# Kernel optimization log

Hardware: AMD Instinct MI355X
Metric: run time of the kernel (lower is better)

## Reference

```python
import jax, jax.numpy as jnp
import numpy as np

D_IN = 6      # raw node feature dim (self_attn_init first arg)
D_INIT = 16   # init encoding dim (self_attn_init second arg)
D_CAT = 22    # 6 + 16 (self_attn_enc first arg)
D_ENC = 64    # encoding dim (self_attn_enc second arg / gated_aggr_attn)
N = 1024      # number of nodes in node_cloud


def setup_inputs() -> dict:
    key = jax.random.key(0)
    ks = jax.random.split(key, 8)
    return {
        "node_cloud": jax.random.normal(ks[0], (N, D_IN), jnp.float32),
        "Wq_i": jax.random.normal(ks[1], (D_IN, D_INIT), jnp.float32) / np.sqrt(D_IN),
        "Wk_i": jax.random.normal(ks[2], (D_IN, D_INIT), jnp.float32) / np.sqrt(D_IN),
        "Wv_i": jax.random.normal(ks[3], (D_IN, D_INIT), jnp.float32) / np.sqrt(D_IN),
        "Wq_e": jax.random.normal(ks[4], (D_IN, D_ENC), jnp.float32) / np.sqrt(D_IN),
        "Wk_e": jax.random.normal(ks[5], (D_CAT, D_ENC), jnp.float32) / np.sqrt(D_CAT),
        "Wv_e": jax.random.normal(ks[6], (D_CAT, D_ENC), jnp.float32) / np.sqrt(D_CAT),
        "wg": jax.random.normal(ks[7], (D_ENC,), jnp.float32) / np.sqrt(D_ENC),
        "bg": jnp.zeros((), jnp.float32),
    }


def reference(node_cloud, Wq_i, Wk_i, Wv_i, Wq_e, Wk_e, Wv_e, wg, bg):
    # Stage 1: self_attn_init, batched over all C=N centres at once.
    # Per centre c: attend over every node, per-node 16-d encoding.
    Q_i = node_cloud @ Wq_i                     # [C, 16] (one query per centre)
    K_i = node_cloud @ Wk_i                     # [N, 16]
    V_i = node_cloud @ Wv_i                     # [N, 16]
    scores_i = (Q_i @ K_i.T) / np.sqrt(D_INIT)  # [C, N]
    a_i = jax.nn.softmax(scores_i, axis=-1)     # [C, N]
    nce_init = a_i[:, :, None] * V_i[None]      # [C, N, 16]

    # Stage 2: self_attn_enc on concat(raw node feats, init encodings).
    x = jnp.concatenate(
        [jnp.broadcast_to(node_cloud[None], (N, N, D_IN)), nce_init], axis=-1
    )                                            # [C, N, 22]
    Q_e = node_cloud @ Wq_e                      # [C, 64]
    K_e = jnp.einsum("cnf,fd->cnd", x, Wk_e)     # [C, N, 64]
    V_e = jnp.einsum("cnf,fd->cnd", x, Wv_e)     # [C, N, 64]
    scores_e = jnp.einsum("cnd,cd->cn", K_e, Q_e) / np.sqrt(D_ENC)  # [C, N]
    a_e = jax.nn.softmax(scores_e, axis=-1)      # [C, N]
    enc = a_e[:, :, None] * V_e                  # [C, N, 64]

    # Stage 3: gated_aggr_attn over the node axis -> one 64-vector per centre.
    g = jax.nn.sigmoid(enc @ wg + bg)            # [C, N]
    out = jnp.einsum("cn,cnd->cd", g, enc)       # [C, 64]
    return out
```

## Files before the change

kernel.cpp:

```cpp
#include <hip/hip_runtime.h>
#include <math.h>

#define NN 1024
#define DE 64
#define DCAT 22
#define GC 2
#define NTC 512
#define NWAVE (NTC/64)
#define NBLK (NN/GC)

__device__ __forceinline__ float wave_sum(float v) {
    int t;
    t = __builtin_amdgcn_update_dpp(0, __float_as_int(v), 0x111, 0xf, 0xf, true); v += __int_as_float(t);
    t = __builtin_amdgcn_update_dpp(0, __float_as_int(v), 0x112, 0xf, 0xf, true); v += __int_as_float(t);
    t = __builtin_amdgcn_update_dpp(0, __float_as_int(v), 0x114, 0xf, 0xf, true); v += __int_as_float(t);
    t = __builtin_amdgcn_update_dpp(0, __float_as_int(v), 0x118, 0xf, 0xf, true); v += __int_as_float(t);
    t = __builtin_amdgcn_update_dpp(0, __float_as_int(v), 0x142, 0xf, 0xf, true); v += __int_as_float(t);
    t = __builtin_amdgcn_update_dpp(0, __float_as_int(v), 0x143, 0xf, 0xf, true); v += __int_as_float(t);
    return v;
}

__global__ __launch_bounds__(NTC, 4) void nce_fused(
    const float* __restrict__ nc,
    const float* __restrict__ Wq_i, const float* __restrict__ Wk_i,
    const float* __restrict__ Wv_i, const float* __restrict__ Wq_e,
    const float* __restrict__ Wk_e, const float* __restrict__ Wv_e,
    const float* __restrict__ wg,  const float* __restrict__ bgp,
    float* __restrict__ out)
{
    __shared__ float  s_wqi[96], s_wki[96], s_wvi[96], s_wg[64];
    __shared__ float  s_wqe[384], s_wke[1408], s_wve[1408];
    __shared__ float  s_M[6*DCAT], s_Mi[36], s_u[DCAT];
    __shared__ float  s_q[GC][32];
    __shared__ float2 s_red1[NWAVE], s_red2[NWAVE];
    __shared__ float2 s_acc[NWAVE][DCAT];
    __shared__ float  s_fin[DCAT*GC];

    const int tid  = threadIdx.x, wave = tid >> 6, lane = tid & 63;
    const int c0   = blockIdx.x * GC;
    const int nA   = tid, nB = tid + NTC;

    float xA[6], xB[6];
    #pragma unroll
    for (int f = 0; f < 6; ++f) { xA[f] = nc[nA*6 + f]; xB[f] = nc[nB*6 + f]; }

    if (tid < 96) { s_wqi[tid] = Wq_i[tid]; s_wki[tid] = Wk_i[tid]; s_wvi[tid] = Wv_i[tid]; }
    else if (tid >= 128 && tid < 192) s_wg[tid-128] = wg[tid-128];
    if (tid < 384) s_wqe[tid] = Wq_e[tid];
    for (int i = tid; i < 1408; i += NTC) { s_wke[i] = Wk_e[i]; s_wve[i] = Wv_e[i]; }
    __syncthreads();

    if (tid < 132) {
        const int f = tid % 6, k = tid / 6;
        float a = 0.f;
        #pragma unroll
        for (int d = 0; d < 64; ++d) a += s_wqe[f*64+d]*s_wke[k*64+d];
        s_M[f*DCAT+k] = a * 0.125f;
    } else if (tid < 168) {
        const int t = tid - 132, g = t % 6, f = t / 6;
        float a = 0.f;
        #pragma unroll
        for (int j = 0; j < 16; ++j) a += s_wqi[g*16+j]*s_wki[f*16+j];
        s_Mi[g*6+f] = a * 0.25f;
    } else if (tid < 190) {
        const int k = tid - 168;
        float a = 0.f;
        #pragma unroll
        for (int d = 0; d < 64; ++d) a += s_wve[k*64+d]*s_wg[d];
        s_u[k] = a;
    }
    __syncthreads();

    float viA[16], viB[16];
    #pragma unroll
    for (int j = 0; j < 16; ++j) {
        float a = 0.f, b = 0.f;
        #pragma unroll
        for (int f = 0; f < 6; ++f) { a += xA[f]*s_wvi[f*16+j]; b += xB[f]*s_wvi[f*16+j]; }
        viA[j] = a; viB[j] = b;
    }
    float grA = 0.f, grB = 0.f, gvA = 0.f, gvB = 0.f;
    #pragma unroll
    for (int f = 0; f < 6; ++f)  { grA += xA[f]*s_u[f];    grB += xB[f]*s_u[f]; }
    #pragma unroll
    for (int j = 0; j < 16; ++j) { gvA += viA[j]*s_u[6+j]; gvB += viB[j]*s_u[6+j]; }

    if (tid < GC*32) {
        const int c = tid >> 5, k = tid & 31;
        float xc[6];
        #pragma unroll
        for (int f = 0; f < 6; ++f) xc[f] = nc[(c0+c)*6 + f];
        float a = 0.f;
        if (k < 6) {
            #pragma unroll
            for (int g = 0; g < 6; ++g) a += xc[g]*s_Mi[g*6+k];
        } else if (k >= 8 && k < 14) {
            #pragma unroll
            for (int f = 0; f < 6; ++f) a += xc[f]*s_M[f*DCAT + (k-8)];
        } else if (k >= 16) {
            #pragma unroll
            for (int f = 0; f < 6; ++f) a += xc[f]*s_M[f*DCAT + 6 + (k-16)];
        }
        s_q[c][k] = a;
    }
    const float bg = *bgp;
    __syncthreads();

    float aiA[GC], aiB[GC];
    #pragma unroll
    for (int c = 0; c < GC; ++c) {
        const float* q = s_q[c];
        float sA = 0.f, sB = 0.f;
        #pragma unroll
        for (int f = 0; f < 6; ++f) { sA += q[f]*xA[f]; sB += q[f]*xB[f]; }
        aiA[c] = __expf(sA); aiB[c] = __expf(sB);
    }
    {
        float r0 = wave_sum(aiA[0]+aiB[0]);
        float r1 = wave_sum(aiA[1]+aiB[1]);
        if (lane == 63) s_red1[wave] = make_float2(r0, r1);
    }
    __syncthreads();
    {
        float2 dd = s_red1[0];
        #pragma unroll
        for (int w2 = 1; w2 < NWAVE; ++w2) { float2 t = s_red1[w2]; dd.x += t.x; dd.y += t.y; }
        float inv0 = 1.f/dd.x, inv1 = 1.f/dd.y;
        aiA[0] *= inv0; aiB[0] *= inv0; aiA[1] *= inv1; aiB[1] *= inv1;
    }

    float w1A[GC], w2A[GC], w1B[GC], w2B[GC];
    {
        float eA[GC], eB[GC];
        #pragma unroll
        for (int c = 0; c < GC; ++c) {
            const float* q = s_q[c];
            float uA = 0.f, uB = 0.f, vA = 0.f, vB = 0.f;
            #pragma unroll
            for (int f = 0; f < 6; ++f) { uA += q[8+f]*xA[f]; uB += q[8+f]*xB[f]; }
            #pragma unroll
            for (int j = 0; j < 16; ++j) { vA += q[16+j]*viA[j]; vB += q[16+j]*viB[j]; }
            eA[c] = __expf(uA + aiA[c]*vA);
            eB[c] = __expf(uB + aiB[c]*vB);
        }
        float s0 = wave_sum(eA[0]+eB[0]);
        float s1 = wave_sum(eA[1]+eB[1]);
        if (lane == 63) s_red2[wave] = make_float2(s0, s1);
        __syncthreads();
        float2 dd = s_red2[0];
        #pragma unroll
        for (int w2 = 1; w2 < NWAVE; ++w2) { float2 t = s_red2[w2]; dd.x += t.x; dd.y += t.y; }
        float den[GC] = {dd.x, dd.y};
        #pragma unroll
        for (int c = 0; c < GC; ++c) {
            float inv = 1.f/den[c];
            float aeA = eA[c]*inv, aeB = eB[c]*inv;
            float preA = aeA*(grA + aiA[c]*gvA) + bg;
            float preB = aeB*(grB + aiB[c]*gvB) + bg;
            float gA = 1.f/(1.f + __expf(-preA));
            float gB = 1.f/(1.f + __expf(-preB));
            w1A[c] = gA*aeA; w2A[c] = w1A[c]*aiA[c];
            w1B[c] = gB*aeB; w2B[c] = w1B[c]*aiB[c];
        }
    }

    #pragma unroll
    for (int f = 0; f < 6; ++f) {
        float a0 = wave_sum(w1A[0]*xA[f] + w1B[0]*xB[f]);
        float a1 = wave_sum(w1A[1]*xA[f] + w1B[1]*xB[f]);
        if (lane == 63) s_acc[wave][f] = make_float2(a0, a1);
    }
    #pragma unroll
    for (int j = 0; j < 16; ++j) {
        float a0 = wave_sum(w2A[0]*viA[j] + w2B[0]*viB[j]);
        float a1 = wave_sum(w2A[1]*viA[j] + w2B[1]*viB[j]);
        if (lane == 63) s_acc[wave][6+j] = make_float2(a0, a1);
    }
    __syncthreads();
    if (tid < DCAT*GC) {
        const int k = tid >> 1, c = tid & 1;
        float a = 0.f;
        #pragma unroll
        for (int w2 = 0; w2 < NWAVE; ++w2)
            a += ((const float*)&s_acc[w2][k])[c];
        s_fin[k*GC + c] = a;
    }
    __syncthreads();

    if (tid < GC*DE) {
        const int c = tid >> 6, d = tid & 63;
        float o = 0.f;
        #pragma unroll
        for (int k = 0; k < DCAT; ++k) o += s_fin[k*GC + c]*s_wve[k*64 + d];
        out[(c0 + c)*DE + d] = o;
    }
}

extern "C" void kernel_launch(void* const* d_in, const int* in_sizes, int n_in,
                              void* d_out, int out_size, void* d_ws, size_t ws_size,
                              hipStream_t stream)
{
    const float* nc   = (const float*)d_in[0];
    const float* Wq_i = (const float*)d_in[1];
    const float* Wk_i = (const float*)d_in[2];
    const float* Wv_i = (const float*)d_in[3];
    const float* Wq_e = (const float*)d_in[4];
    const float* Wk_e = (const float*)d_in[5];
    const float* Wv_e = (const float*)d_in[6];
    const float* wg   = (const float*)d_in[7];
    const float* bg   = (const float*)d_in[8];
    float* out = (float*)d_out;

    nce_fused<<<NBLK, NTC, 0, stream>>>(nc, Wq_i, Wk_i, Wv_i, Wq_e, Wk_e, Wv_e,
                                        wg, bg, out);
}
```

Baseline: 21.63 us.

## Split weight-product and per-node precompute into a prologue kernel

Adds a small pre-kernel that computes the folded weight matrices (M, Mi, u), a transposed copy of the node features and the per-node V_i values, and stores them in workspace. The main per-centre kernel then loads these instead of having every one of 512 blocks redo the weight products and V_i projection. It also switches the final reductions to 16-lane DPP sums with a wider shared partial array, and uses float4 reads of the query vectors. The cost is a second kernel launch and a serial dependency between the two kernels.

```diff
diff --git a/kernel.cpp b/kernel.cpp
--- a/kernel.cpp
+++ b/kernel.cpp
@@ -8,6 +8,12 @@
 #define NTC 512
 #define NWAVE (NTC/64)
 #define NBLK (NN/GC)
+
+#define OFF_M   0
+#define OFF_MI  132
+#define OFF_U   168
+#define OFF_XT  192
+#define OFF_VIT (OFF_XT + 6*NN)
 
 __device__ __forceinline__ float wave_sum(float v) {
     int t;
@@ -19,100 +25,125 @@
     t = __builtin_amdgcn_update_dpp(0, __float_as_int(v), 0x143, 0xf, 0xf, true); v += __int_as_float(t);
     return v;
 }
-
-__global__ __launch_bounds__(NTC, 4) void nce_fused(
+__device__ __forceinline__ float wave_sum16(float v) {
+    int t;
+    t = __builtin_amdgcn_update_dpp(0, __float_as_int(v), 0x111, 0xf, 0xf, true); v += __int_as_float(t);
+    t = __builtin_amdgcn_update_dpp(0, __float_as_int(v), 0x112, 0xf, 0xf, true); v += __int_as_float(t);
+    t = __builtin_amdgcn_update_dpp(0, __float_as_int(v), 0x114, 0xf, 0xf, true); v += __int_as_float(t);
+    t = __builtin_amdgcn_update_dpp(0, __float_as_int(v), 0x118, 0xf, 0xf, true); v += __int_as_float(t);
+    return v;
+}
+
+__global__ __launch_bounds__(256) void nce_pre(
     const float* __restrict__ nc,
     const float* __restrict__ Wq_i, const float* __restrict__ Wk_i,
     const float* __restrict__ Wv_i, const float* __restrict__ Wq_e,
     const float* __restrict__ Wk_e, const float* __restrict__ Wv_e,
-    const float* __restrict__ wg,  const float* __restrict__ bgp,
+    const float* __restrict__ wg, float* __restrict__ ws)
+{
+    __shared__ float s_wqi[96], s_wki[96], s_wvi[96], s_wg[64];
+    __shared__ float s_wqe[384], s_wke[1408], s_wve[1408];
+    const int tid = threadIdx.x, bid = blockIdx.x;
+    const int wv = tid >> 6, lane = tid & 63;
+
+    if (tid < 96) { s_wqi[tid] = Wq_i[tid]; s_wki[tid] = Wk_i[tid]; s_wvi[tid] = Wv_i[tid]; }
+    if (tid >= 96 && tid < 160) s_wg[tid-96] = wg[tid-96];
+    for (int i = tid; i < 384; i += 256) s_wqe[i] = Wq_e[i];
+    for (int i = tid; i < 1408; i += 256) { s_wke[i] = Wk_e[i]; s_wve[i] = Wv_e[i]; }
+    __syncthreads();
+
+    for (int e = bid*4 + wv; e < 190; e += 16) {
+        float p; int dst; float scale;
+        if (e < 132) {
+            const int f = e % 6, k = e / 6;
+            p = s_wqe[f*64 + lane] * s_wke[k*64 + lane];
+            dst = OFF_M + f*22 + k; scale = 0.125f;
+        } else if (e < 168) {
+            const int t = e - 132, g = t % 6, f = t / 6;
+            p = (lane < 16) ? s_wqi[g*16 + lane] * s_wki[f*16 + lane] : 0.f;
+            dst = OFF_MI + g*6 + f; scale = 0.25f;
+        } else {
+            const int k = e - 168;
+            p = s_wve[k*64 + lane] * s_wg[lane];
+            dst = OFF_U + k; scale = 1.f;
+        }
+        float ssum = wave_sum(p);
+        if (lane == 63) ws[dst] = ssum * scale;
+    }
+
+    const int n = bid*256 + tid;
+    float x[6];
+    #pragma unroll
+    for (int f = 0; f < 6; ++f) { x[f] = nc[n*6 + f]; ws[OFF_XT + f*NN + n] = x[f]; }
+    #pragma unroll
+    for (int j = 0; j < 16; ++j) {
+        float a = 0.f;
+        #pragma unroll
+        for (int f = 0; f < 6; ++f) a += x[f]*s_wvi[f*16 + j];
+        ws[OFF_VIT + j*NN + n] = a;
+    }
+}
+
+__global__ __launch_bounds__(NTC, 4) void nce_centre(
+    const float* __restrict__ ws, const float* __restrict__ nc,
+    const float* __restrict__ Wv_e, const float* __restrict__ bgp,
     float* __restrict__ out)
 {
-    __shared__ float  s_wqi[96], s_wki[96], s_wvi[96], s_wg[64];
-    __shared__ float  s_wqe[384], s_wke[1408], s_wve[1408];
-    __shared__ float  s_M[6*DCAT], s_Mi[36], s_u[DCAT];
-    __shared__ float  s_q[GC][32];
+    __shared__ float  s_c[192];
+    __shared__ float  s_wve[DCAT*DE];
+    __shared__ __align__(16) float s_q[GC][32];
     __shared__ float2 s_red1[NWAVE], s_red2[NWAVE];
-    __shared__ float2 s_acc[NWAVE][DCAT];
+    __shared__ float2 s_acc[32][DCAT];
     __shared__ float  s_fin[DCAT*GC];
 
-    const int tid  = threadIdx.x, wave = tid >> 6, lane = tid & 63;
-    const int c0   = blockIdx.x * GC;
-    const int nA   = tid, nB = tid + NTC;
-
-    float xA[6], xB[6];
-    #pragma unroll
-    for (int f = 0; f < 6; ++f) { xA[f] = nc[nA*6 + f]; xB[f] = nc[nB*6 + f]; }
-
-    if (tid < 96) { s_wqi[tid] = Wq_i[tid]; s_wki[tid] = Wk_i[tid]; s_wvi[tid] = Wv_i[tid]; }
-    else if (tid >= 128 && tid < 192) s_wg[tid-128] = wg[tid-128];
-    if (tid < 384) s_wqe[tid] = Wq_e[tid];
-    for (int i = tid; i < 1408; i += NTC) { s_wke[i] = Wk_e[i]; s_wve[i] = Wv_e[i]; }
-    __syncthreads();
-
-    if (tid < 132) {
-        const int f = tid % 6, k = tid / 6;
-        float a = 0.f;
-        #pragma unroll
-        for (int d = 0; d < 64; ++d) a += s_wqe[f*64+d]*s_wke[k*64+d];
-        s_M[f*DCAT+k] = a * 0.125f;
-    } else if (tid < 168) {
-        const int t = tid - 132, g = t % 6, f = t / 6;
-        float a = 0.f;
-        #pragma unroll
-        for (int j = 0; j < 16; ++j) a += s_wqi[g*16+j]*s_wki[f*16+j];
-        s_Mi[g*6+f] = a * 0.25f;
-    } else if (tid < 190) {
-        const int k = tid - 168;
-        float a = 0.f;
-        #pragma unroll
-        for (int d = 0; d < 64; ++d) a += s_wve[k*64+d]*s_wg[d];
-        s_u[k] = a;
-    }
-    __syncthreads();
-
-    float viA[16], viB[16];
-    #pragma unroll
-    for (int j = 0; j < 16; ++j) {
-        float a = 0.f, b = 0.f;
-        #pragma unroll
-        for (int f = 0; f < 6; ++f) { a += xA[f]*s_wvi[f*16+j]; b += xB[f]*s_wvi[f*16+j]; }
-        viA[j] = a; viB[j] = b;
-    }
-    float grA = 0.f, grB = 0.f, gvA = 0.f, gvB = 0.f;
-    #pragma unroll
-    for (int f = 0; f < 6; ++f)  { grA += xA[f]*s_u[f];    grB += xB[f]*s_u[f]; }
-    #pragma unroll
-    for (int j = 0; j < 16; ++j) { gvA += viA[j]*s_u[6+j]; gvB += viB[j]*s_u[6+j]; }
+    const int tid = threadIdx.x, wave = tid >> 6, lane = tid & 63;
+    const int c0 = blockIdx.x * GC;
+    const int nA = tid, nB = tid + NTC;
+
+    float xA[6], xB[6], viA[16], viB[16];
+    #pragma unroll
+    for (int f = 0; f < 6; ++f) { xA[f] = ws[OFF_XT + f*NN + nA]; xB[f] = ws[OFF_XT + f*NN + nB]; }
+    #pragma unroll
+    for (int j = 0; j < 16; ++j) { viA[j] = ws[OFF_VIT + j*NN + nA]; viB[j] = ws[OFF_VIT + j*NN + nB]; }
+
+    if (tid < 192) s_c[tid] = (tid < 190) ? ws[tid] : 0.f;
+    if (tid < 352) ((float4*)s_wve)[tid] = ((const float4*)Wv_e)[tid];
+    if (tid >= 448) ((float*)s_q)[tid-448] = 0.f;
+    const float bg = *bgp;
+    __syncthreads();
 
     if (tid < GC*32) {
         const int c = tid >> 5, k = tid & 31;
         float xc[6];
         #pragma unroll
         for (int f = 0; f < 6; ++f) xc[f] = nc[(c0+c)*6 + f];
-        float a = 0.f;
+        float a = 0.f; bool live = true;
         if (k < 6) {
             #pragma unroll
-            for (int g = 0; g < 6; ++g) a += xc[g]*s_Mi[g*6+k];
+            for (int g = 0; g < 6; ++g) a += xc[g]*s_c[OFF_MI + g*6 + k];
         } else if (k >= 8 && k < 14) {
             #pragma unroll
-            for (int f = 0; f < 6; ++f) a += xc[f]*s_M[f*DCAT + (k-8)];
+            for (int f = 0; f < 6; ++f) a += xc[f]*s_c[OFF_M + f*22 + (k-8)];
         } else if (k >= 16) {
             #pragma unroll
-            for (int f = 0; f < 6; ++f) a += xc[f]*s_M[f*DCAT + 6 + (k-16)];
-        }
-        s_q[c][k] = a;
-    }
-    const float bg = *bgp;
+            for (int f = 0; f < 6; ++f) a += xc[f]*s_c[OFF_M + f*22 + 6 + (k-16)];
+        } else live = false;
+        if (live) s_q[c][k] = a;
+    }
+    float grA = 0.f, grB = 0.f, gvA = 0.f, gvB = 0.f;
+    #pragma unroll
+    for (int f = 0; f < 6; ++f)  { grA += xA[f]*s_c[OFF_U + f];    grB += xB[f]*s_c[OFF_U + f]; }
+    #pragma unroll
+    for (int j = 0; j < 16; ++j) { gvA += viA[j]*s_c[OFF_U + 6+j]; gvB += viB[j]*s_c[OFF_U + 6+j]; }
     __syncthreads();
 
     float aiA[GC], aiB[GC];
     #pragma unroll
     for (int c = 0; c < GC; ++c) {
-        const float* q = s_q[c];
-        float sA = 0.f, sB = 0.f;
-        #pragma unroll
-        for (int f = 0; f < 6; ++f) { sA += q[f]*xA[f]; sB += q[f]*xB[f]; }
+        const float4* q4 = (const float4*)s_q[c];
+        float4 q0 = q4[0], q1 = q4[1];
+        float sA = q0.x*xA[0] + q0.y*xA[1] + q0.z*xA[2] + q0.w*xA[3] + q1.x*xA[4] + q1.y*xA[5];
+        float sB = q0.x*xB[0] + q0.y*xB[1] + q0.z*xB[2] + q0.w*xB[3] + q1.x*xB[4] + q1.y*xB[5];
         aiA[c] = __expf(sA); aiB[c] = __expf(sB);
     }
     {
@@ -134,12 +165,17 @@
         float eA[GC], eB[GC];
         #pragma unroll
         for (int c = 0; c < GC; ++c) {
-            const float* q = s_q[c];
-            float uA = 0.f, uB = 0.f, vA = 0.f, vB = 0.f;
-            #pragma unroll
-            for (int f = 0; f < 6; ++f) { uA += q[8+f]*xA[f]; uB += q[8+f]*xB[f]; }
-            #pragma unroll
-            for (int j = 0; j < 16; ++j) { vA += q[16+j]*viA[j]; vB += q[16+j]*viB[j]; }
+            const float4* q4 = (const float4*)s_q[c];
+            float4 q2 = q4[2], q3 = q4[3];
+            float uA = q2.x*xA[0] + q2.y*xA[1] + q2.z*xA[2] + q2.w*xA[3] + q3.x*xA[4] + q3.y*xA[5];
+            float uB = q2.x*xB[0] + q2.y*xB[1] + q2.z*xB[2] + q2.w*xB[3] + q3.x*xB[4] + q3.y*xB[5];
+            float vA = 0.f, vB = 0.f;
+            #pragma unroll
+            for (int h = 0; h < 4; ++h) {
+                float4 qq = q4[4+h];
+                vA += qq.x*viA[h*4+0] + qq.y*viA[h*4+1] + qq.z*viA[h*4+2] + qq.w*viA[h*4+3];
+                vB += qq.x*viB[h*4+0] + qq.y*viB[h*4+1] + qq.z*viB[h*4+2] + qq.w*viB[h*4+3];
+            }
             eA[c] = __expf(uA + aiA[c]*vA);
             eB[c] = __expf(uB + aiB[c]*vB);
         }
@@ -164,25 +200,25 @@
         }
     }
 
+    const int row = (wave << 2) + (lane >> 4);
     #pragma unroll
     for (int f = 0; f < 6; ++f) {
-        float a0 = wave_sum(w1A[0]*xA[f] + w1B[0]*xB[f]);
-        float a1 = wave_sum(w1A[1]*xA[f] + w1B[1]*xB[f]);
-        if (lane == 63) s_acc[wave][f] = make_float2(a0, a1);
+        float a0 = wave_sum16(w1A[0]*xA[f] + w1B[0]*xB[f]);
+        float a1 = wave_sum16(w1A[1]*xA[f] + w1B[1]*xB[f]);
+        if ((lane & 15) == 15) s_acc[row][f] = make_float2(a0, a1);
     }
     #pragma unroll
     for (int j = 0; j < 16; ++j) {
-        float a0 = wave_sum(w2A[0]*viA[j] + w2B[0]*viB[j]);
-        float a1 = wave_sum(w2A[1]*viA[j] + w2B[1]*viB[j]);
-        if (lane == 63) s_acc[wave][6+j] = make_float2(a0, a1);
+        float a0 = wave_sum16(w2A[0]*viA[j] + w2B[0]*viB[j]);
+        float a1 = wave_sum16(w2A[1]*viA[j] + w2B[1]*viB[j]);
+        if ((lane & 15) == 15) s_acc[row][6+j] = make_float2(a0, a1);
     }
     __syncthreads();
     if (tid < DCAT*GC) {
         const int k = tid >> 1, c = tid & 1;
         float a = 0.f;
         #pragma unroll
-        for (int w2 = 0; w2 < NWAVE; ++w2)
-            a += ((const float*)&s_acc[w2][k])[c];
+        for (int r = 0; r < 32; ++r) a += ((const float*)&s_acc[r][k])[c];
         s_fin[k*GC + c] = a;
     }
     __syncthreads();
@@ -210,7 +246,8 @@
     const float* wg   = (const float*)d_in[7];
     const float* bg   = (const float*)d_in[8];
     float* out = (float*)d_out;
-
-    nce_fused<<<NBLK, NTC, 0, stream>>>(nc, Wq_i, Wk_i, Wv_i, Wq_e, Wk_e, Wv_e,
-                                        wg, bg, out);
-}
+    float* ws  = (float*)d_ws;
+
+    nce_pre<<<4, 256, 0, stream>>>(nc, Wq_i, Wk_i, Wv_i, Wq_e, Wk_e, Wv_e, wg, ws);
+    nce_centre<<<NBLK, NTC, 0, stream>>>(ws, nc, Wv_e, bg, out);
+}
```

Result: faster. 19.84 us (-8.2%).
